# Performance work log

Measured on AMD Instinct MI355X. Metric: run time of the kernel, lower is better.

The kernel has to match this reference:

```python
import jax, jax.numpy as jnp
import numpy as np

EPS = 1e-12  # torch F.normalize clamp
D = 4        # max_displacement


def _l2norm_c(x):
    # L2 normalize over channel dim (axis=1), matching F.normalize(p=2, dim=1)
    n = jnp.sqrt(jnp.sum(x * x, axis=1, keepdims=True))
    return x / jnp.maximum(n, EPS)


def setup_inputs() -> dict:
    key = jax.random.key(0)
    k1, k2 = jax.random.split(key)
    B, C, H, W = 4, 128, 128, 256
    feat1 = jax.random.normal(k1, (B, C, H, W), dtype=jnp.float32)
    feat2_warped = jax.random.normal(k2, (B, C, H, W), dtype=jnp.float32)
    return {"feat1": feat1, "feat2_warped": feat2_warped}


def reference(feat1, feat2_warped):
    B, C, H, W = feat1.shape
    f1 = _l2norm_c(feat1)
    f2 = _l2norm_c(feat2_warped)
    # zero-pad spatial dims by D (matches F.unfold padding=D)
    f2p = jnp.pad(f2, ((0, 0), (0, 0), (D, D), (D, D)))
    costs = []
    # fixed (2D+1)^2 = 81 displacements, row-major (dy, dx) to match unfold ordering
    for dy in range(2 * D + 1):
        for dx in range(2 * D + 1):
            shifted = jax.lax.slice(f2p, (0, 0, dy, dx), (B, C, dy + H, dx + W))
            costs.append(jnp.sum(f1 * shifted, axis=1) / C)  # (B,H,W)
    cost = jnp.stack(costs, axis=1)  # (B, 81, H, W)
    return jax.nn.leaky_relu(cost, negative_slope=0.1)
```

## Files before the change

### kernel.cpp

```cpp
#include <hip/hip_runtime.h>

#define B_ 4
#define C_ 128
#define H_ 128
#define W_ 256
#define HW_ (H_ * W_)
#define ND 81
#define TH 8
#define TW 16
#define HR 16
#define WCOL 32
#define KC 32
#define NCHUNK (C_ / KC)
#define NTHREADS 512

typedef short bf16x8 __attribute__((ext_vector_type(8)));
typedef float f32x4 __attribute__((ext_vector_type(4)));
typedef float f32x4v __attribute__((ext_vector_type(4)));
typedef unsigned int u32x4 __attribute__((ext_vector_type(4)));

__device__ __forceinline__ int swz(int px, int byteInHalf) {
    int r = px >> 1;
    int base = (r << 7) + ((px & 1) << 6) + byteInHalf;
    return base ^ ((r & 7) << 4);
}

__device__ __forceinline__ unsigned int cvt_pk_bf16(float a, float b) {
    unsigned int r;
    asm("v_cvt_pk_bf16_f32 %0, %1, %2" : "=v"(r) : "v"(a), "v"(b));
    return r;
}

__device__ __forceinline__ void dot2_sq(unsigned int u, float& ss) {
    asm("v_dot2_f32_bf16 %0, %1, %1, %0" : "+v"(ss) : "v"(u));
}

#define BARRIER()                                             \
    do {                                                      \
        asm volatile("s_waitcnt lgkmcnt(0)" ::: "memory");    \
        __builtin_amdgcn_s_barrier();                         \
    } while (0)

__global__ __launch_bounds__(NTHREADS)
void corr81_kernel(const float* __restrict__ f1g, const float* __restrict__ f2g,
                   float* __restrict__ out) {
    __shared__ __align__(16) unsigned short f2s[2][HR * WCOL * KC];
    __shared__ __align__(16) unsigned short f1s[2][TH * TW * KC];
    float* invn2 = (float*)&f2s[0][0];
    float* invn1 = (float*)&f1s[0][0];

    const int tid  = threadIdx.x;
    const int lane = tid & 63;
    const int wave = tid >> 6;
    const int col  = lane & 15;
    const int quad = lane >> 4;

    const int flat = blockIdx.x + 16 * blockIdx.y + 256 * blockIdx.z;
    const int orig = (flat & 7) * 128 + (flat >> 3);
    const int w0 = (orig & 15) * TW;
    const int h0 = ((orig >> 4) & 15) * TH;
    const int b  = orig >> 8;
    const size_t inBase = (size_t)b * C_ * HW_;
    const float* f2base = f2g + inBase;
    const float* f1base = f1g + inBase;

    const int g2  = tid & 7;
    const int cp2 = (tid >> 3) & 15;
    const int rq  = tid >> 7;
    const int gw2 = w0 - 4 + g2 * 4;
    const bool colok2 = (gw2 >= 0) && (gw2 < W_);

    const int g1  = tid & 3;
    const int cp1 = (tid >> 2) & 15;
    const int r1  = tid >> 6;

    bool vrow[4];
    int off2[4];
#pragma unroll
    for (int i = 0; i < 4; ++i) {
        int r  = i * 4 + rq;
        int gh = h0 - 4 + r;
        vrow[i] = colok2 && (gh >= 0) && (gh < H_);
        off2[i] = cp2 * 2 * HW_ + (vrow[i] ? (gh * W_ + gw2) : 0);
    }
    const int off1 = cp1 * 2 * HW_ + (h0 + r1) * W_ + (w0 + g1 * 4);

    const int rb2 = swz(wave * 32 + col, quad * 16);
    const int rb1 = swz(wave * 16 + col, quad * 16);
    const char* f2c = (const char*)&f2s[0][0];
    const char* f1c = (const char*)&f1s[0][0];

    f32x4 acc[9][2];
#pragma unroll
    for (int d = 0; d < 9; ++d) {
        acc[d][0] = (f32x4)0.f;
        acc[d][1] = (f32x4)0.f;
    }

    float ss2 = 0.f, ss1 = 0.f;
    f32x4v A0[4] = {}, A1[4] = {}, B0, B1;

#define ISSUE_LOADS(kc0)                                                        \
    {                                                                           \
        const float* bk2 = f2base + (size_t)(kc0) * HW_;                        \
        const float* bk1 = f1base + (size_t)(kc0) * HW_;                        \
        _Pragma("unroll")                                                       \
        for (int i = 0; i < 4; ++i) {                                           \
            if (vrow[i]) {                                                      \
                A0[i] = *(const f32x4v*)(bk2 + off2[i]);                        \
                A1[i] = *(const f32x4v*)(bk2 + off2[i] + HW_);                  \
            }                                                                   \
        }                                                                       \
        B0 = *(const f32x4v*)(bk1 + off1);                                      \
        B1 = *(const f32x4v*)(bk1 + off1 + HW_);                                \
    }

#define PACK_WRITE(buf)                                                         \
    {                                                                           \
        char* w2 = (char*)&f2s[(buf)][0];                                       \
        char* w1 = (char*)&f1s[(buf)][0];                                       \
        _Pragma("unroll")                                                       \
        for (int i = 0; i < 4; ++i) {                                           \
            int r = i * 4 + rq;                                                 \
            _Pragma("unroll")                                                   \
            for (int j = 0; j < 4; ++j) {                                       \
                int px = r * 32 + g2 * 4 + j;                                   \
                *(unsigned int*)(w2 + swz(px, cp2 * 4)) =                       \
                    cvt_pk_bf16(A0[i][j], A1[i][j]);                            \
            }                                                                   \
        }                                                                       \
        _Pragma("unroll")                                                       \
        for (int j = 0; j < 4; ++j) {                                           \
            int px = r1 * 16 + g1 * 4 + j;                                      \
            *(unsigned int*)(w1 + swz(px, cp1 * 4)) = cvt_pk_bf16(B0[j], B1[j]);\
        }                                                                       \
    }

#define MFMA_PHASE(buf)                                                         \
    {                                                                           \
        bf16x8 af = *(const bf16x8*)(f1c + rb1 + (buf) * 8192);                 \
        _Pragma("unroll")                                                       \
        for (int dy = 0; dy < 9; ++dy) {                                        \
            bf16x8 b0 = *(const bf16x8*)(f2c + rb2 + (buf) * 32768 + dy * 2048);\
            bf16x8 b1 = *(const bf16x8*)(f2c + rb2 + (buf) * 32768 + dy * 2048 + 1024); \
            acc[dy][0] = __builtin_amdgcn_mfma_f32_16x16x32_bf16(af, b0, acc[dy][0], 0, 0, 0); \
            acc[dy][1] = __builtin_amdgcn_mfma_f32_16x16x32_bf16(af, b1, acc[dy][1], 0, 0, 0); \
        }                                                                       \
    }

#define NORM_PHASE(buf)                                                         \
    {                                                                           \
        const char* r2 = (const char*)&f2s[(buf)][0];                           \
        const char* r1p = (const char*)&f1s[(buf)][0];                          \
        _Pragma("unroll")                                                       \
        for (int j = 0; j < 4; ++j) {                                           \
            u32x4 v = *(const u32x4*)(r2 + swz(tid, j * 16));                   \
            dot2_sq(v[0], ss2); dot2_sq(v[1], ss2);                             \
            dot2_sq(v[2], ss2); dot2_sq(v[3], ss2);                             \
        }                                                                       \
        u32x4 v = *(const u32x4*)(r1p + swz(tid >> 2, (tid & 3) * 16));         \
        dot2_sq(v[0], ss1); dot2_sq(v[1], ss1);                                 \
        dot2_sq(v[2], ss1); dot2_sq(v[3], ss1);                                 \
    }

    ISSUE_LOADS(0);
    PACK_WRITE(0);
    ISSUE_LOADS(KC);
    BARRIER();

#pragma unroll
    for (int k = 0; k < NCHUNK; ++k) {
        const int bk = k & 1;
        MFMA_PHASE(bk);
        if (k < NCHUNK - 1) {
            PACK_WRITE(bk ^ 1);
            if (k < NCHUNK - 2) ISSUE_LOADS((k + 2) * KC);
            NORM_PHASE(bk);
        } else {
            NORM_PHASE(bk);
            invn2[tid] = 1.f / fmaxf(sqrtf(ss2), 1e-12f);
            float t1 = ss1 + __shfl_xor(ss1, 1);
            t1 += __shfl_xor(t1, 2);
            if ((tid & 3) == 0) invn1[tid >> 2] = 1.f / fmaxf(sqrtf(t1), 1e-12f);
        }
        BARRIER();
    }

    const int hOut = h0 + wave;
    float* outB = out + (size_t)b * ND * HW_ + (size_t)hOut * W_;
    const float scale = 1.f / (float)C_;

#pragma unroll
    for (int dy = 0; dy < 9; ++dy) {
        int hr = wave + dy;
#pragma unroll
        for (int t = 0; t < 2; ++t) {
            float i2 = invn2[hr * WCOL + t * 16 + col];
#pragma unroll
            for (int r = 0; r < 4; ++r) {
                int row = quad * 4 + r;
                int dx = t * 16 + col - row;
                if (dx >= 0 && dx <= 8) {
                    float v = acc[dy][t][r] * invn1[wave * 16 + row] * i2 * scale;
                    v = (v >= 0.f) ? v : 0.1f * v;
                    outB[(size_t)(dy * 9 + dx) * HW_ + (w0 + row)] = v;
                }
            }
        }
    }
#undef ISSUE_LOADS
#undef PACK_WRITE
#undef MFMA_PHASE
#undef NORM_PHASE
}

extern "C" void kernel_launch(void* const* d_in, const int* in_sizes, int n_in,
                              void* d_out, int out_size, void* d_ws, size_t ws_size,
                              hipStream_t stream) {
    const float* f1 = (const float*)d_in[0];
    const float* f2 = (const float*)d_in[1];
    float* out = (float*)d_out;
    dim3 grid(W_ / TW, H_ / TH, B_);
    corr81_kernel<<<grid, NTHREADS, 0, stream>>>(f1, f2, out);
}
```

Before: 64.58 us.

## Single-buffer LDS staging to cut shared memory and raise occupancy

Replaces the double-buffered bf16 LDS tiles with a single buffer and gives the inverse norms their own small arrays. Each chunk now runs MFMA and norm reads, then a barrier, then packs the next chunk and issues the following global loads, then a second barrier. This roughly halves LDS use, which may let more blocks fit per CU. In exchange it adds a barrier per chunk and serialises the LDS writes with the MFMA phase, so compute and LDS packing no longer overlap within a block.

```diff
diff --git a/kernel.cpp b/kernel.cpp
--- a/kernel.cpp
+++ b/kernel.cpp
@@ -44,10 +44,10 @@
 __global__ __launch_bounds__(NTHREADS)
 void corr81_kernel(const float* __restrict__ f1g, const float* __restrict__ f2g,
                    float* __restrict__ out) {
-    __shared__ __align__(16) unsigned short f2s[2][HR * WCOL * KC];
-    __shared__ __align__(16) unsigned short f1s[2][TH * TW * KC];
-    float* invn2 = (float*)&f2s[0][0];
-    float* invn1 = (float*)&f1s[0][0];
+    __shared__ __align__(16) unsigned short f2s[HR * WCOL * KC];
+    __shared__ __align__(16) unsigned short f1s[TH * TW * KC];
+    __shared__ float invn2[HR * WCOL];
+    __shared__ float invn1[TH * TW];
 
     const int tid  = threadIdx.x;
     const int lane = tid & 63;
@@ -87,8 +87,8 @@
 
     const int rb2 = swz(wave * 32 + col, quad * 16);
     const int rb1 = swz(wave * 16 + col, quad * 16);
-    const char* f2c = (const char*)&f2s[0][0];
-    const char* f1c = (const char*)&f1s[0][0];
+    const char* f2c = (const char*)&f2s[0];
+    const char* f1c = (const char*)&f1s[0];
 
     f32x4 acc[9][2];
 #pragma unroll
@@ -115,10 +115,10 @@
         B1 = *(const f32x4v*)(bk1 + off1 + HW_);                                \
     }
 
-#define PACK_WRITE(buf)                                                         \
-    {                                                                           \
-        char* w2 = (char*)&f2s[(buf)][0];                                       \
-        char* w1 = (char*)&f1s[(buf)][0];                                       \
+#define PACK_WRITE()                                                            \
+    {                                                                           \
+        char* w2 = (char*)&f2s[0];                                              \
+        char* w1 = (char*)&f1s[0];                                              \
         _Pragma("unroll")                                                       \
         for (int i = 0; i < 4; ++i) {                                           \
             int r = i * 4 + rq;                                                 \
@@ -136,54 +136,52 @@
         }                                                                       \
     }
 
-#define MFMA_PHASE(buf)                                                         \
-    {                                                                           \
-        bf16x8 af = *(const bf16x8*)(f1c + rb1 + (buf) * 8192);                 \
+#define MFMA_PHASE()                                                            \
+    {                                                                           \
+        bf16x8 af = *(const bf16x8*)(f1c + rb1);                                \
         _Pragma("unroll")                                                       \
         for (int dy = 0; dy < 9; ++dy) {                                        \
-            bf16x8 b0 = *(const bf16x8*)(f2c + rb2 + (buf) * 32768 + dy * 2048);\
-            bf16x8 b1 = *(const bf16x8*)(f2c + rb2 + (buf) * 32768 + dy * 2048 + 1024); \
+            bf16x8 b0 = *(const bf16x8*)(f2c + rb2 + dy * 2048);                \
+            bf16x8 b1 = *(const bf16x8*)(f2c + rb2 + dy * 2048 + 1024);         \
             acc[dy][0] = __builtin_amdgcn_mfma_f32_16x16x32_bf16(af, b0, acc[dy][0], 0, 0, 0); \
             acc[dy][1] = __builtin_amdgcn_mfma_f32_16x16x32_bf16(af, b1, acc[dy][1], 0, 0, 0); \
         }                                                                       \
     }
 
-#define NORM_PHASE(buf)                                                         \
-    {                                                                           \
-        const char* r2 = (const char*)&f2s[(buf)][0];                           \
-        const char* r1p = (const char*)&f1s[(buf)][0];                          \
+#define NORM_PHASE()                                                            \
+    {                                                                           \
         _Pragma("unroll")                                                       \
         for (int j = 0; j < 4; ++j) {                                           \
-            u32x4 v = *(const u32x4*)(r2 + swz(tid, j * 16));                   \
+            u32x4 v = *(const u32x4*)(f2c + swz(tid, j * 16));                  \
             dot2_sq(v[0], ss2); dot2_sq(v[1], ss2);                             \
             dot2_sq(v[2], ss2); dot2_sq(v[3], ss2);                             \
         }                                                                       \
-        u32x4 v = *(const u32x4*)(r1p + swz(tid >> 2, (tid & 3) * 16));         \
+        u32x4 v = *(const u32x4*)(f1c + swz(tid >> 2, (tid & 3) * 16));         \
         dot2_sq(v[0], ss1); dot2_sq(v[1], ss1);                                 \
         dot2_sq(v[2], ss1); dot2_sq(v[3], ss1);                                 \
     }
 
     ISSUE_LOADS(0);
-    PACK_WRITE(0);
+    PACK_WRITE();
     ISSUE_LOADS(KC);
     BARRIER();
 
 #pragma unroll
     for (int k = 0; k < NCHUNK; ++k) {
-        const int bk = k & 1;
-        MFMA_PHASE(bk);
-        if (k < NCHUNK - 1) {
-            PACK_WRITE(bk ^ 1);
-            if (k < NCHUNK - 2) ISSUE_LOADS((k + 2) * KC);
-            NORM_PHASE(bk);
-        } else {
-            NORM_PHASE(bk);
+        MFMA_PHASE();
+        NORM_PHASE();
+        if (k == NCHUNK - 1) {
             invn2[tid] = 1.f / fmaxf(sqrtf(ss2), 1e-12f);
             float t1 = ss1 + __shfl_xor(ss1, 1);
             t1 += __shfl_xor(t1, 2);
             if ((tid & 3) == 0) invn1[tid >> 2] = 1.f / fmaxf(sqrtf(t1), 1e-12f);
         }
         BARRIER();
+        if (k < NCHUNK - 1) {
+            PACK_WRITE();
+            if (k < NCHUNK - 2) ISSUE_LOADS((k + 2) * KC);
+            BARRIER();
+        }
     }
 
     const int hOut = h0 + wave;
```

After: 66.87 us. 3.6% more time.
